# Kernel tuning notes

Hardware: AMD Instinct MI355X
Metric: run time of the kernel (lower is better)

Reference implementation:

```python
import jax, jax.numpy as jnp
import numpy as np


def l2norm(t, eps=1e-12):
    # matches F.normalize(p=2, dim=-1): divide by norm clamped to eps
    n = jnp.linalg.norm(t, axis=-1, keepdims=True)
    return t / jnp.maximum(n, eps)


def setup_inputs() -> dict:
    key = jax.random.key(0)
    kx, ke = jax.random.split(key)
    B, N, D, C = 8, 1024, 256, 8192
    x = jax.random.normal(kx, (B, N, D), dtype=jnp.float32)
    # codebook initialized l2-normalized, as in __init__ (kmeans_init=False)
    embed = l2norm(jax.random.normal(ke, (1, C, D), dtype=jnp.float32))
    return {"x": x, "embed": embed}


def reference(x, embed):
    # x: [B, N, D]; ndim < 4 -> add codebook dim h=1
    xh = x[None]                                   # [1, B, N, D]
    h, b, n, d = xh.shape
    flat = l2norm(xh.reshape(h, b * n, d))         # [1, B*N, D]
    e = l2norm(embed)                              # [1, C, D]
    # cosine-similarity distances
    dist = jnp.einsum('hnd,hcd->hnc', flat, e)     # [1, B*N, C]
    # sample_codebook_temp == 0 -> plain argmax
    idx = jnp.argmax(dist, axis=-1).reshape(h, b, n)  # [1, B, N]
    # batched_embedding: gather UN-normalized codebook rows
    quantize = jax.vmap(lambda em, ix: em[ix])(embed, idx)  # [1, B, N, D]
    # needs_codebook_dim -> strip leading dim
    return quantize[0], idx[0]
```

## Files before the change

kernel.cpp:

```cpp
#include <hip/hip_runtime.h>
#include <math.h>

#define QROWS 8192
#define DDIM  256
#define CCNT  8192
#define BM    128
#define BN    128
#define BK    32
#define CBLKS (CCNT / BN)
#define KSTEPS (DDIM / BK)

typedef __attribute__((ext_vector_type(4))) float f32x4;
typedef __attribute__((ext_vector_type(8))) short bf16x8;

__device__ __forceinline__ unsigned short f2bf(float f) {
    unsigned u = __float_as_uint(f);
    u += 0x7fffu + ((u >> 16) & 1u);
    return (unsigned short)(u >> 16);
}
__device__ __forceinline__ unsigned u32max(unsigned a, unsigned b) { return a > b ? a : b; }
__device__ __forceinline__ unsigned u32min(unsigned a, unsigned b) { return a < b ? a : b; }

__device__ __forceinline__ unsigned key32(float v, unsigned enc) {
    unsigned u = __float_as_uint(v);
    unsigned s = (unsigned)((int)u >> 31);
    return ((u ^ (s | 0x80000000u)) & 0xFFFFFF80u) | enc;
}

__global__ void k_prep_x(const float* __restrict__ x, unsigned short* __restrict__ xb) {
    const int i = (blockIdx.x * 256 + threadIdx.x) * 8;
    const float4 f0 = *reinterpret_cast<const float4*>(x + i);
    const float4 f1 = *reinterpret_cast<const float4*>(x + i + 4);
    uint4 o;
    o.x = f2bf(f0.x) | ((unsigned)f2bf(f0.y) << 16);
    o.y = f2bf(f0.z) | ((unsigned)f2bf(f0.w) << 16);
    o.z = f2bf(f1.x) | ((unsigned)f2bf(f1.y) << 16);
    o.w = f2bf(f1.z) | ((unsigned)f2bf(f1.w) << 16);
    *reinterpret_cast<uint4*>(xb + i) = o;
}

__global__ void k_prep_e(const float* __restrict__ e, unsigned short* __restrict__ eb) {
    const int row  = blockIdx.x * 4 + (threadIdx.x >> 6);
    const int lane = threadIdx.x & 63;
    const float4 v = *reinterpret_cast<const float4*>(e + (size_t)row * DDIM + lane * 4);
    float s = v.x * v.x + v.y * v.y + v.z * v.z + v.w * v.w;
    #pragma unroll
    for (int off = 1; off < 64; off <<= 1) s += __shfl_xor(s, off);
    const float inv = 1.0f / fmaxf(sqrtf(s), 1e-12f);
    ushort4 o;
    o.x = f2bf(v.x * inv); o.y = f2bf(v.y * inv);
    o.z = f2bf(v.z * inv); o.w = f2bf(v.w * inv);
    *reinterpret_cast<ushort4*>(eb + (size_t)row * DDIM + lane * 4) = o;
}

#define GLOAD_LDS(g, s) \
    __builtin_amdgcn_global_load_lds((const __attribute__((address_space(1))) void*)(g), \
                                     (__attribute__((address_space(3))) void*)(s), 16, 0, 0)

__launch_bounds__(256)
__global__ void k_gemm(const unsigned short* __restrict__ xb,
                       const unsigned short* __restrict__ eb,
                       unsigned* pout ) {
    __shared__ __align__(16) char smem[33792];

    const int tid = threadIdx.x;
    const int w = tid >> 6, l = tid & 63;
    const int wr = w >> 1, wc = w & 1;
    const int lg = l >> 4, lr = l & 15;
    const int bx = blockIdx.x, by = blockIdx.y;
    const int n0 = by * BM, c0 = bx * BN;

    const f32x4 zero = {0.f, 0.f, 0.f, 0.f};
    f32x4 acc[4][4];
    #pragma unroll
    for (int i = 0; i < 4; ++i)
        #pragma unroll
        for (int j = 0; j < 4; ++j) acc[i][j] = zero;

    const char* gA = (const char*)xb + (size_t)(n0 + (tid >> 2)) * 512 + (tid & 3) * 16;
    const char* gB = (const char*)eb + (size_t)(c0 + (tid >> 2)) * 512 + (tid & 3) * 16;
    const int wb = w * 1024;

    #define STAGE(buf, s) do {                                         \
        const int kb_ = (s) * 64;                                      \
        char* Ab_ = smem + (buf) * 8192 + wb;                          \
        char* Bb_ = smem + 16384 + (buf) * 8192 + wb;                  \
        GLOAD_LDS(gA + kb_, Ab_);                                      \
        GLOAD_LDS(gA + 64 * 512 + kb_, Ab_ + 4096);                    \
        GLOAD_LDS(gB + kb_, Bb_);                                      \
        GLOAD_LDS(gB + 64 * 512 + kb_, Bb_ + 4096);                    \
    } while (0)

    STAGE(0, 0);
    __syncthreads();

    #pragma unroll
    for (int s = 0; s < KSTEPS; ++s) {
        const int cur = s & 1;
        if (s + 1 < KSTEPS) STAGE(cur ^ 1, s + 1);

        const unsigned short* At = (const unsigned short*)(smem + cur * 8192);
        const unsigned short* Bt = (const unsigned short*)(smem + 16384 + cur * 8192);
        bf16x8 a[4], b[4];
        const int koff = lg * 8;
        #pragma unroll
        for (int mi = 0; mi < 4; ++mi)
            a[mi] = *reinterpret_cast<const bf16x8*>(&At[(wr * 64 + mi * 16 + lr) * BK + koff]);
        #pragma unroll
        for (int nj = 0; nj < 4; ++nj)
            b[nj] = *reinterpret_cast<const bf16x8*>(&Bt[(wc * 64 + nj * 16 + lr) * BK + koff]);
        #pragma unroll
        for (int mi = 0; mi < 4; ++mi)
            #pragma unroll
            for (int nj = 0; nj < 4; ++nj)
                acc[mi][nj] = __builtin_amdgcn_mfma_f32_16x16x32_bf16(a[mi], b[nj], acc[mi][nj], 0, 0, 0);
        __syncthreads();
    }

    uint2* T = (uint2*)smem;
    const unsigned encbase = (unsigned)(127 - wc * 64 - lr);
    #pragma unroll
    for (int mi = 0; mi < 4; ++mi) {
        #pragma unroll
        for (int r = 0; r < 4; ++r) {
            unsigned k0 = key32(acc[mi][0][r], encbase);
            unsigned k1 = key32(acc[mi][1][r], encbase - 16);
            unsigned k2 = key32(acc[mi][2][r], encbase - 32);
            unsigned k3 = key32(acc[mi][3][r], encbase - 48);
            const unsigned m01 = u32max(k0, k1), n01 = u32min(k0, k1);
            const unsigned m23 = u32max(k2, k3), n23 = u32min(k2, k3);
            const unsigned t1 = u32max(m01, m23);
            const unsigned t2 = u32max(u32min(m01, m23), u32max(n01, n23));
            const int rloc = wr * 64 + mi * 16 + lg * 4 + r;
            uint2 p; p.x = t1; p.y = t2;
            T[rloc * 33 + wc * 16 + lr] = p;
        }
    }
    __syncthreads();

    if (tid < BM) {
        const uint2* rp = T + tid * 33;
        unsigned T1 = 0, T2 = 0;
        #pragma unroll
        for (int i = 0; i < 32; ++i) {
            const uint2 p = rp[i];
            const unsigned n1 = u32max(T1, p.x);
            const unsigned lo = u32min(T1, p.x);
            T2 = u32max(T2, u32max(lo, p.y));
            T1 = n1;
        }
        uint2 o; o.x = T1; o.y = T2;
        *reinterpret_cast<uint2*>(pout + (size_t)(n0 + tid) * 256 + bx * 2) = o;
    }
    #undef STAGE
}

__device__ __forceinline__ unsigned long long expand_key(unsigned k, int blk) {
    const int col = blk * 128 + 127 - (int)(k & 127u);
    return ((unsigned long long)(k & 0xFFFFFF80u) << 32) | (unsigned)(~col);
}

__global__ void k_fixup(const unsigned* pk,
                        const float* __restrict__ x, const float* __restrict__ e,
                        float* out) {
    const int row = blockIdx.x;
    const int t   = threadIdx.x;
    const uint2 kv = reinterpret_cast<const uint2*>(pk + (size_t)row * 256)[t];
    unsigned long long kk0 = expand_key(kv.x, t);
    unsigned long long kk1 = expand_key(kv.y, t);

    int cand[4];
    #pragma unroll
    for (int p = 0; p < 4; ++p) {
        unsigned long long m = kk0 > kk1 ? kk0 : kk1;
        #pragma unroll
        for (int off = 1; off < 64; off <<= 1) {
            const unsigned long long o = __shfl_xor(m, off);
            if (o > m) m = o;
        }
        cand[p] = (int)(~(unsigned)m) & (CCNT - 1);
        if (kk0 == m) kk0 = 0ull;
        if (kk1 == m) kk1 = 0ull;
    }

    const float4 xv = *reinterpret_cast<const float4*>(x + (size_t)row * DDIM + t * 4);
    float best = -INFINITY; int bc = 0x7fffffff;
    #pragma unroll
    for (int p = 0; p < 4; ++p) {
        const int c = cand[p];
        const float4 ev = *reinterpret_cast<const float4*>(e + (size_t)c * DDIM + t * 4);
        float d  = xv.x * ev.x + xv.y * ev.y + xv.z * ev.z + xv.w * ev.w;
        float ss = ev.x * ev.x + ev.y * ev.y + ev.z * ev.z + ev.w * ev.w;
        #pragma unroll
        for (int off = 1; off < 64; off <<= 1) {
            d  += __shfl_xor(d, off);
            ss += __shfl_xor(ss, off);
        }
        const float v = d * (1.0f / fmaxf(sqrtf(ss), 1e-12f));
        if (v > best || (v == best && c < bc)) { best = v; bc = c; }
    }

    if (t == 0) out[(size_t)QROWS * DDIM + row] = (float)bc;
    const float4 q = *reinterpret_cast<const float4*>(e + (size_t)bc * DDIM + t * 4);
    *reinterpret_cast<float4*>(out + (size_t)row * DDIM + t * 4) = q;
}

extern "C" void kernel_launch(void* const* d_in, const int* in_sizes, int n_in,
                              void* d_out, int out_size, void* d_ws, size_t ws_size,
                              hipStream_t stream) {
    const float* x = (const float*)d_in[0];
    const float* e = (const float*)d_in[1];
    float* out = (float*)d_out;
    char* ws = (char*)d_ws;

    unsigned short* xb = (unsigned short*)ws;
    unsigned short* eb = (unsigned short*)(ws + (size_t)4 * 1024 * 1024);

    k_prep_x<<<QROWS * DDIM / (256 * 8), 256, 0, stream>>>(x, xb);
    k_prep_e<<<CCNT / 4, 256, 0, stream>>>(e, eb);
    dim3 g2(CBLKS, QROWS / BM);
    k_gemm<<<g2, 256, 0, stream>>>(xb, eb, (unsigned*)d_out);
    k_fixup<<<QROWS, 64, 0, stream>>>((const unsigned*)d_out, x, e, out);
}
```

Measured before the change: 71.41 us.

## Deepen GEMM K-tile with swizzled LDS, manual waitcnt pipeline, merge prep kernels

The GEMM now stages 64-wide K tiles with an XOR-swizzled LDS layout to avoid bank conflicts. The K loop is fully unrolled into a hand-scheduled double-buffered pipeline using explicit vmcnt/lgkmcnt waits, raw barriers and setprio around the MFMA blocks. The two prep kernels are merged into one launch, and the fixup kernel packs four rows per 256-thread block. The intent is to cut barrier count, LDS conflicts and launch overhead, at the cost of doubling LDS to 64KB, which may lower occupancy.

New measurement: 65.54 us. 8.2% less time.

```diff
diff --git a/kernel.cpp b/kernel.cpp
--- a/kernel.cpp
+++ b/kernel.cpp
@@ -6,9 +6,8 @@
 #define CCNT  8192
 #define BM    128
 #define BN    128
-#define BK    32
+#define BK    64
 #define CBLKS (CCNT / BN)
-#define KSTEPS (DDIM / BK)
 
 typedef __attribute__((ext_vector_type(4))) float f32x4;
 typedef __attribute__((ext_vector_type(8))) short bf16x8;
@@ -27,41 +26,52 @@
     return ((u ^ (s | 0x80000000u)) & 0xFFFFFF80u) | enc;
 }
 
-__global__ void k_prep_x(const float* __restrict__ x, unsigned short* __restrict__ xb) {
-    const int i = (blockIdx.x * 256 + threadIdx.x) * 8;
-    const float4 f0 = *reinterpret_cast<const float4*>(x + i);
-    const float4 f1 = *reinterpret_cast<const float4*>(x + i + 4);
-    uint4 o;
-    o.x = f2bf(f0.x) | ((unsigned)f2bf(f0.y) << 16);
-    o.y = f2bf(f0.z) | ((unsigned)f2bf(f0.w) << 16);
-    o.z = f2bf(f1.x) | ((unsigned)f2bf(f1.y) << 16);
-    o.w = f2bf(f1.z) | ((unsigned)f2bf(f1.w) << 16);
-    *reinterpret_cast<uint4*>(xb + i) = o;
-}
-
-__global__ void k_prep_e(const float* __restrict__ e, unsigned short* __restrict__ eb) {
-    const int row  = blockIdx.x * 4 + (threadIdx.x >> 6);
-    const int lane = threadIdx.x & 63;
-    const float4 v = *reinterpret_cast<const float4*>(e + (size_t)row * DDIM + lane * 4);
-    float s = v.x * v.x + v.y * v.y + v.z * v.z + v.w * v.w;
-    #pragma unroll
-    for (int off = 1; off < 64; off <<= 1) s += __shfl_xor(s, off);
-    const float inv = 1.0f / fmaxf(sqrtf(s), 1e-12f);
-    ushort4 o;
-    o.x = f2bf(v.x * inv); o.y = f2bf(v.y * inv);
-    o.z = f2bf(v.z * inv); o.w = f2bf(v.w * inv);
-    *reinterpret_cast<ushort4*>(eb + (size_t)row * DDIM + lane * 4) = o;
+__global__ void k_prep(const float* __restrict__ x, unsigned short* __restrict__ xb,
+                       const float* __restrict__ e, unsigned short* __restrict__ eb) {
+    const int bid = blockIdx.x;
+    if (bid < 1024) {
+        const int i = (bid * 256 + threadIdx.x) * 8;
+        const float4 f0 = *reinterpret_cast<const float4*>(x + i);
+        const float4 f1 = *reinterpret_cast<const float4*>(x + i + 4);
+        uint4 o;
+        o.x = f2bf(f0.x) | ((unsigned)f2bf(f0.y) << 16);
+        o.y = f2bf(f0.z) | ((unsigned)f2bf(f0.w) << 16);
+        o.z = f2bf(f1.x) | ((unsigned)f2bf(f1.y) << 16);
+        o.w = f2bf(f1.z) | ((unsigned)f2bf(f1.w) << 16);
+        *reinterpret_cast<uint4*>(xb + i) = o;
+    } else {
+        const int row  = (bid - 1024) * 4 + (threadIdx.x >> 6);
+        const int lane = threadIdx.x & 63;
+        const float4 v = *reinterpret_cast<const float4*>(e + (size_t)row * DDIM + lane * 4);
+        float s = v.x * v.x + v.y * v.y + v.z * v.z + v.w * v.w;
+        #pragma unroll
+        for (int off = 1; off < 64; off <<= 1) s += __shfl_xor(s, off);
+        const float inv = 1.0f / fmaxf(sqrtf(s), 1e-12f);
+        ushort4 o;
+        o.x = f2bf(v.x * inv); o.y = f2bf(v.y * inv);
+        o.z = f2bf(v.z * inv); o.w = f2bf(v.w * inv);
+        *reinterpret_cast<ushort4*>(eb + (size_t)row * DDIM + lane * 4) = o;
+    }
 }
 
 #define GLOAD_LDS(g, s) \
     __builtin_amdgcn_global_load_lds((const __attribute__((address_space(1))) void*)(g), \
                                      (__attribute__((address_space(3))) void*)(s), 16, 0, 0)
+
+#define SBAR do { asm volatile("" ::: "memory"); __builtin_amdgcn_s_barrier(); \
+                  asm volatile("" ::: "memory"); } while (0)
+#define WAIT_LGKM0 do { asm volatile("s_waitcnt lgkmcnt(0)" ::: "memory"); \
+                        __builtin_amdgcn_sched_barrier(0); } while (0)
+#define WAIT_VM8 do { asm volatile("s_waitcnt vmcnt(8)" ::: "memory"); \
+                      __builtin_amdgcn_sched_barrier(0); } while (0)
+#define WAIT_VM0 do { asm volatile("s_waitcnt vmcnt(0)" ::: "memory"); \
+                      __builtin_amdgcn_sched_barrier(0); } while (0)
 
 __launch_bounds__(256)
 __global__ void k_gemm(const unsigned short* __restrict__ xb,
                        const unsigned short* __restrict__ eb,
                        unsigned* pout ) {
-    __shared__ __align__(16) char smem[33792];
+    __shared__ __align__(16) char smem[65536];
 
     const int tid = threadIdx.x;
     const int w = tid >> 6, l = tid & 63;
@@ -77,45 +87,71 @@
         #pragma unroll
         for (int j = 0; j < 4; ++j) acc[i][j] = zero;
 
-    const char* gA = (const char*)xb + (size_t)(n0 + (tid >> 2)) * 512 + (tid & 3) * 16;
-    const char* gB = (const char*)eb + (size_t)(c0 + (tid >> 2)) * 512 + (tid & 3) * 16;
+    const int srow = tid >> 3;
+    const int swzp = (tid & 7) ^ (srow & 7);
+    const char* gA = (const char*)xb + (size_t)(n0 + srow) * 512 + swzp * 16;
+    const char* gB = (const char*)eb + (size_t)(c0 + srow) * 512 + swzp * 16;
     const int wb = w * 1024;
 
-    #define STAGE(buf, s) do {                                         \
-        const int kb_ = (s) * 64;                                      \
-        char* Ab_ = smem + (buf) * 8192 + wb;                          \
-        char* Bb_ = smem + 16384 + (buf) * 8192 + wb;                  \
-        GLOAD_LDS(gA + kb_, Ab_);                                      \
-        GLOAD_LDS(gA + 64 * 512 + kb_, Ab_ + 4096);                    \
-        GLOAD_LDS(gB + kb_, Bb_);                                      \
-        GLOAD_LDS(gB + 64 * 512 + kb_, Bb_ + 4096);                    \
-    } while (0)
-
-    STAGE(0, 0);
+#define STAGE(Ab, Bb, kb) do {                                          \
+    GLOAD_LDS(gA + (kb),         smem + (Ab) + 0 * 4096 + wb);          \
+    GLOAD_LDS(gA + (kb) + 16384, smem + (Ab) + 1 * 4096 + wb);          \
+    GLOAD_LDS(gA + (kb) + 32768, smem + (Ab) + 2 * 4096 + wb);          \
+    GLOAD_LDS(gA + (kb) + 49152, smem + (Ab) + 3 * 4096 + wb);          \
+    GLOAD_LDS(gB + (kb),         smem + (Bb) + 0 * 4096 + wb);          \
+    GLOAD_LDS(gB + (kb) + 16384, smem + (Bb) + 1 * 4096 + wb);          \
+    GLOAD_LDS(gB + (kb) + 32768, smem + (Bb) + 2 * 4096 + wb);          \
+    GLOAD_LDS(gB + (kb) + 49152, smem + (Bb) + 3 * 4096 + wb);          \
+} while (0)
+
+    const int aoff = (wr * 64 + lr) * 128;
+    const int boff = (wc * 64 + lr) * 128;
+    const int k0 = ((0 + lg) ^ (lr & 7)) * 16;
+    const int k1 = ((4 + lg) ^ (lr & 7)) * 16;
+
+    bf16x8 a[4][2], b[4][2];
+#define READS(Ab, Bb) do {                                                           \
+    _Pragma("unroll") for (int mi = 0; mi < 4; ++mi) {                               \
+        a[mi][0] = *reinterpret_cast<const bf16x8*>(smem + (Ab) + aoff + mi * 2048 + k0); \
+        a[mi][1] = *reinterpret_cast<const bf16x8*>(smem + (Ab) + aoff + mi * 2048 + k1); \
+    }                                                                                \
+    _Pragma("unroll") for (int nj = 0; nj < 4; ++nj) {                               \
+        b[nj][0] = *reinterpret_cast<const bf16x8*>(smem + (Bb) + boff + nj * 2048 + k0); \
+        b[nj][1] = *reinterpret_cast<const bf16x8*>(smem + (Bb) + boff + nj * 2048 + k1); \
+    }                                                                                \
+} while (0)
+
+#define MMAS() do {                                                     \
+    __builtin_amdgcn_s_setprio(1);                                      \
+    _Pragma("unroll") for (int kk = 0; kk < 2; ++kk)                    \
+      _Pragma("unroll") for (int mi = 0; mi < 4; ++mi)                  \
+        _Pragma("unroll") for (int nj = 0; nj < 4; ++nj)                \
+          acc[mi][nj] = __builtin_amdgcn_mfma_f32_16x16x32_bf16(a[mi][kk], b[nj][kk], acc[mi][nj], 0, 0, 0); \
+    __builtin_amdgcn_s_setprio(0);                                      \
+} while (0)
+
+    STAGE(0, 32768, 0);
+    STAGE(16384, 49152, 128);
+    WAIT_VM8; SBAR;
+
+    READS(0, 32768);
+    WAIT_LGKM0; SBAR;
+    STAGE(0, 32768, 256);
+    MMAS();
+    WAIT_VM8; SBAR;
+    READS(16384, 49152);
+    WAIT_LGKM0; SBAR;
+    STAGE(16384, 49152, 384);
+    MMAS();
+    WAIT_VM8; SBAR;
+    READS(0, 32768);
+    WAIT_LGKM0; SBAR;
+    MMAS();
+    WAIT_VM0; SBAR;
+    READS(16384, 49152);
+    WAIT_LGKM0;
+    MMAS();
     __syncthreads();
-
-    #pragma unroll
-    for (int s = 0; s < KSTEPS; ++s) {
-        const int cur = s & 1;
-        if (s + 1 < KSTEPS) STAGE(cur ^ 1, s + 1);
-
-        const unsigned short* At = (const unsigned short*)(smem + cur * 8192);
-        const unsigned short* Bt = (const unsigned short*)(smem + 16384 + cur * 8192);
-        bf16x8 a[4], b[4];
-        const int koff = lg * 8;
-        #pragma unroll
-        for (int mi = 0; mi < 4; ++mi)
-            a[mi] = *reinterpret_cast<const bf16x8*>(&At[(wr * 64 + mi * 16 + lr) * BK + koff]);
-        #pragma unroll
-        for (int nj = 0; nj < 4; ++nj)
-            b[nj] = *reinterpret_cast<const bf16x8*>(&Bt[(wc * 64 + nj * 16 + lr) * BK + koff]);
-        #pragma unroll
-        for (int mi = 0; mi < 4; ++mi)
-            #pragma unroll
-            for (int nj = 0; nj < 4; ++nj)
-                acc[mi][nj] = __builtin_amdgcn_mfma_f32_16x16x32_bf16(a[mi], b[nj], acc[mi][nj], 0, 0, 0);
-        __syncthreads();
-    }
 
     uint2* T = (uint2*)smem;
     const unsigned encbase = (unsigned)(127 - wc * 64 - lr);
@@ -123,12 +159,12 @@
     for (int mi = 0; mi < 4; ++mi) {
         #pragma unroll
         for (int r = 0; r < 4; ++r) {
-            unsigned k0 = key32(acc[mi][0][r], encbase);
-            unsigned k1 = key32(acc[mi][1][r], encbase - 16);
-            unsigned k2 = key32(acc[mi][2][r], encbase - 32);
-            unsigned k3 = key32(acc[mi][3][r], encbase - 48);
-            const unsigned m01 = u32max(k0, k1), n01 = u32min(k0, k1);
-            const unsigned m23 = u32max(k2, k3), n23 = u32min(k2, k3);
+            unsigned q0 = key32(acc[mi][0][r], encbase);
+            unsigned q1 = key32(acc[mi][1][r], encbase - 16);
+            unsigned q2 = key32(acc[mi][2][r], encbase - 32);
+            unsigned q3 = key32(acc[mi][3][r], encbase - 48);
+            const unsigned m01 = u32max(q0, q1), n01 = u32min(q0, q1);
+            const unsigned m23 = u32max(q2, q3), n23 = u32min(q2, q3);
             const unsigned t1 = u32max(m01, m23);
             const unsigned t2 = u32max(u32min(m01, m23), u32max(n01, n23));
             const int rloc = wr * 64 + mi * 16 + lg * 4 + r;
@@ -152,7 +188,9 @@
         uint2 o; o.x = T1; o.y = T2;
         *reinterpret_cast<uint2*>(pout + (size_t)(n0 + tid) * 256 + bx * 2) = o;
     }
-    #undef STAGE
+#undef STAGE
+#undef READS
+#undef MMAS
 }
 
 __device__ __forceinline__ unsigned long long expand_key(unsigned k, int blk) {
@@ -163,8 +201,8 @@
 __global__ void k_fixup(const unsigned* pk,
                         const float* __restrict__ x, const float* __restrict__ e,
                         float* out) {
-    const int row = blockIdx.x;
-    const int t   = threadIdx.x;
+    const int row = blockIdx.x * 4 + (threadIdx.x >> 6);
+    const int t   = threadIdx.x & 63;
     const uint2 kv = reinterpret_cast<const uint2*>(pk + (size_t)row * 256)[t];
     unsigned long long kk0 = expand_key(kv.x, t);
     unsigned long long kk1 = expand_key(kv.y, t);
@@ -216,9 +254,8 @@
     unsigned short* xb = (unsigned short*)ws;
     unsigned short* eb = (unsigned short*)(ws + (size_t)4 * 1024 * 1024);
 
-    k_prep_x<<<QROWS * DDIM / (256 * 8), 256, 0, stream>>>(x, xb);
-    k_prep_e<<<CCNT / 4, 256, 0, stream>>>(e, eb);
+    k_prep<<<3072, 256, 0, stream>>>(x, xb, e, eb);
     dim3 g2(CBLKS, QROWS / BM);
     k_gemm<<<g2, 256, 0, stream>>>(xb, eb, (unsigned*)d_out);
-    k_fixup<<<QROWS, 64, 0, stream>>>((const unsigned*)d_out, x, e, out);
-}
+    k_fixup<<<QROWS / 4, 256, 0, stream>>>((const unsigned*)d_out, x, e, out);
+}
```

## Rewrite GEMM as persistent 512x512 tiles with register-resident A and streamed top-2 reduction

Applied to the files above, without the earlier changes.

Merges the two prep kernels into one launch. Rewrites the similarity GEMM so each 512-thread block owns a 512-row panel of x and a 512-code slice of the codebook. Each wave keeps its full-depth A fragments in registers while codebook tiles stream through a 4-deep XOR-swizzled LDS ring with explicit waitcnt/barrier scheduling and setprio around the MFMAs. Top-2 keys are reduced on the fly in registers with shuffles, so the LDS epilogue goes away, and the fixup kernel packs 4 rows per block over 32 partials per row. This aims to cut global re-reads of x, launch count and epilogue overhead, at the cost of 128KB LDS, high register pressure and a coarser 8-bit column encoding that drops precision bits from the keys.

Result: faster. 67.46 us (-5.5%).

```diff
diff --git a/kernel.cpp b/kernel.cpp
--- a/kernel.cpp
+++ b/kernel.cpp
@@ -4,11 +4,6 @@
 #define QROWS 8192
 #define DDIM  256
 #define CCNT  8192
-#define BM    128
-#define BN    128
-#define BK    32
-#define CBLKS (CCNT / BN)
-#define KSTEPS (DDIM / BK)
 
 typedef __attribute__((ext_vector_type(4))) float f32x4;
 typedef __attribute__((ext_vector_type(8))) short bf16x8;
@@ -24,150 +19,191 @@
 __device__ __forceinline__ unsigned key32(float v, unsigned enc) {
     unsigned u = __float_as_uint(v);
     unsigned s = (unsigned)((int)u >> 31);
-    return ((u ^ (s | 0x80000000u)) & 0xFFFFFF80u) | enc;
-}
-
-__global__ void k_prep_x(const float* __restrict__ x, unsigned short* __restrict__ xb) {
-    const int i = (blockIdx.x * 256 + threadIdx.x) * 8;
-    const float4 f0 = *reinterpret_cast<const float4*>(x + i);
-    const float4 f1 = *reinterpret_cast<const float4*>(x + i + 4);
-    uint4 o;
-    o.x = f2bf(f0.x) | ((unsigned)f2bf(f0.y) << 16);
-    o.y = f2bf(f0.z) | ((unsigned)f2bf(f0.w) << 16);
-    o.z = f2bf(f1.x) | ((unsigned)f2bf(f1.y) << 16);
-    o.w = f2bf(f1.z) | ((unsigned)f2bf(f1.w) << 16);
-    *reinterpret_cast<uint4*>(xb + i) = o;
-}
-
-__global__ void k_prep_e(const float* __restrict__ e, unsigned short* __restrict__ eb) {
-    const int row  = blockIdx.x * 4 + (threadIdx.x >> 6);
-    const int lane = threadIdx.x & 63;
-    const float4 v = *reinterpret_cast<const float4*>(e + (size_t)row * DDIM + lane * 4);
-    float s = v.x * v.x + v.y * v.y + v.z * v.z + v.w * v.w;
-    #pragma unroll
-    for (int off = 1; off < 64; off <<= 1) s += __shfl_xor(s, off);
-    const float inv = 1.0f / fmaxf(sqrtf(s), 1e-12f);
-    ushort4 o;
-    o.x = f2bf(v.x * inv); o.y = f2bf(v.y * inv);
-    o.z = f2bf(v.z * inv); o.w = f2bf(v.w * inv);
-    *reinterpret_cast<ushort4*>(eb + (size_t)row * DDIM + lane * 4) = o;
+    return ((u ^ (s | 0x80000000u)) & 0xFFFFFF00u) | enc;
+}
+
+__global__ void k_prep(const float* __restrict__ x, unsigned short* __restrict__ xb,
+                       const float* __restrict__ e, unsigned short* __restrict__ eb) {
+    const int bid = blockIdx.x;
+    if (bid < 1024) {
+        const int i = (bid * 256 + threadIdx.x) * 8;
+        const float4 f0 = *reinterpret_cast<const float4*>(x + i);
+        const float4 f1 = *reinterpret_cast<const float4*>(x + i + 4);
+        uint4 o;
+        o.x = f2bf(f0.x) | ((unsigned)f2bf(f0.y) << 16);
+        o.y = f2bf(f0.z) | ((unsigned)f2bf(f0.w) << 16);
+        o.z = f2bf(f1.x) | ((unsigned)f2bf(f1.y) << 16);
+        o.w = f2bf(f1.z) | ((unsigned)f2bf(f1.w) << 16);
+        *reinterpret_cast<uint4*>(xb + i) = o;
+    } else {
+        const int row  = (bid - 1024) * 4 + (threadIdx.x >> 6);
+        const int lane = threadIdx.x & 63;
+        const float4 v = *reinterpret_cast<const float4*>(e + (size_t)row * DDIM + lane * 4);
+        float s = v.x * v.x + v.y * v.y + v.z * v.z + v.w * v.w;
+        #pragma unroll
+        for (int off = 1; off < 64; off <<= 1) s += __shfl_xor(s, off);
+        const float inv = 1.0f / fmaxf(sqrtf(s), 1e-12f);
+        ushort4 o;
+        o.x = f2bf(v.x * inv); o.y = f2bf(v.y * inv);
+        o.z = f2bf(v.z * inv); o.w = f2bf(v.w * inv);
+        *reinterpret_cast<ushort4*>(eb + (size_t)row * DDIM + lane * 4) = o;
+    }
 }
 
 #define GLOAD_LDS(g, s) \
     __builtin_amdgcn_global_load_lds((const __attribute__((address_space(1))) void*)(g), \
                                      (__attribute__((address_space(3))) void*)(s), 16, 0, 0)
 
-__launch_bounds__(256)
+#define SBAR do { asm volatile("" ::: "memory"); __builtin_amdgcn_s_barrier(); \
+                  asm volatile("" ::: "memory"); } while (0)
+#define WAIT_LGKM(n) do { asm volatile("s_waitcnt lgkmcnt(" #n ")" ::: "memory"); \
+                          __builtin_amdgcn_sched_barrier(0); } while (0)
+#define WAIT_VM(n) do { asm volatile("s_waitcnt vmcnt(" #n ")" ::: "memory"); \
+                        __builtin_amdgcn_sched_barrier(0); } while (0)
+
+__launch_bounds__(512, 2)
 __global__ void k_gemm(const unsigned short* __restrict__ xb,
                        const unsigned short* __restrict__ eb,
                        unsigned* pout ) {
-    __shared__ __align__(16) char smem[33792];
+    extern __shared__ char smem[];
 
     const int tid = threadIdx.x;
     const int w = tid >> 6, l = tid & 63;
-    const int wr = w >> 1, wc = w & 1;
     const int lg = l >> 4, lr = l & 15;
-    const int bx = blockIdx.x, by = blockIdx.y;
-    const int n0 = by * BM, c0 = bx * BN;
-
-    const f32x4 zero = {0.f, 0.f, 0.f, 0.f};
-    f32x4 acc[4][4];
-    #pragma unroll
-    for (int i = 0; i < 4; ++i)
-        #pragma unroll
-        for (int j = 0; j < 4; ++j) acc[i][j] = zero;
-
-    const char* gA = (const char*)xb + (size_t)(n0 + (tid >> 2)) * 512 + (tid & 3) * 16;
-    const char* gB = (const char*)eb + (size_t)(c0 + (tid >> 2)) * 512 + (tid & 3) * 16;
-    const int wb = w * 1024;
-
-    #define STAGE(buf, s) do {                                         \
-        const int kb_ = (s) * 64;                                      \
-        char* Ab_ = smem + (buf) * 8192 + wb;                          \
-        char* Bb_ = smem + 16384 + (buf) * 8192 + wb;                  \
-        GLOAD_LDS(gA + kb_, Ab_);                                      \
-        GLOAD_LDS(gA + 64 * 512 + kb_, Ab_ + 4096);                    \
-        GLOAD_LDS(gB + kb_, Bb_);                                      \
-        GLOAD_LDS(gB + 64 * 512 + kb_, Bb_ + 4096);                    \
-    } while (0)
-
-    STAGE(0, 0);
-    __syncthreads();
-
-    #pragma unroll
-    for (int s = 0; s < KSTEPS; ++s) {
-        const int cur = s & 1;
-        if (s + 1 < KSTEPS) STAGE(cur ^ 1, s + 1);
-
-        const unsigned short* At = (const unsigned short*)(smem + cur * 8192);
-        const unsigned short* Bt = (const unsigned short*)(smem + 16384 + cur * 8192);
-        bf16x8 a[4], b[4];
-        const int koff = lg * 8;
-        #pragma unroll
-        for (int mi = 0; mi < 4; ++mi)
-            a[mi] = *reinterpret_cast<const bf16x8*>(&At[(wr * 64 + mi * 16 + lr) * BK + koff]);
-        #pragma unroll
-        for (int nj = 0; nj < 4; ++nj)
-            b[nj] = *reinterpret_cast<const bf16x8*>(&Bt[(wc * 64 + nj * 16 + lr) * BK + koff]);
+    const int bid = blockIdx.x;
+    const int panel = (bid & 7) * 2 + ((bid >> 3) >> 4);
+    const int split = (bid >> 3) & 15;
+    const int n0 = panel * 512, c0 = split * 512;
+
+    const int arl = w * 2 + (l >> 5);
+    const size_t soff = (size_t)(((l & 31) ^ (arl & 7)) * 16);
+    const char* gApro = (const char*)xb + (size_t)(n0 + arl) * 512 + soff;
+    const char* gBpro = (const char*)eb + (size_t)(c0 + arl) * 512 + soff;
+    const int wlds = w * 1024;
+
+#define STAGEA(r) do { _Pragma("unroll") for (int g_ = 0; g_ < 4; ++g_)                    \
+    GLOAD_LDS(gApro + (r) * 32768 + g_ * 8192,                                             \
+              smem + ((r) & 1) * 32768 + g_ * 8192 + wlds); } while (0)
+#define STAGEB(t) do { _Pragma("unroll") for (int g_ = 0; g_ < 2; ++g_)                    \
+    GLOAD_LDS(gBpro + (size_t)(t) * 16384 + g_ * 8192,                                     \
+              smem + 65536 + ((t) & 3) * 16384 + g_ * 8192 + wlds); } while (0)
+
+    bf16x8 aF[4][8];
+#define READA(slot) do { _Pragma("unroll") for (int mi_ = 0; mi_ < 4; ++mi_)               \
+    _Pragma("unroll") for (int kk_ = 0; kk_ < 8; ++kk_)                                    \
+        aF[mi_][kk_] = *reinterpret_cast<const bf16x8*>(smem + (slot) * 32768              \
+            + (mi_ * 16 + lr) * 512 + (((kk_ * 4 + lg) ^ (lr & 7)) * 16)); } while (0)
+
+    STAGEA(0); STAGEA(1);
+    STAGEB(0); STAGEB(1); STAGEB(2); STAGEB(3);
+    WAIT_VM(12); SBAR;  if (w == 0) READA(0);  WAIT_LGKM(0); SBAR; STAGEA(2);
+    WAIT_VM(12); SBAR;  if (w == 1) READA(1);  WAIT_LGKM(0); SBAR; STAGEA(3);
+    WAIT_VM(4);  SBAR;  if (w == 2) READA(0);  WAIT_LGKM(0); SBAR; STAGEA(4);
+    WAIT_VM(4);  SBAR;  if (w == 3) READA(1);  WAIT_LGKM(0); SBAR; STAGEA(5);
+    WAIT_VM(4);  SBAR;  if (w == 4) READA(0);  WAIT_LGKM(0); SBAR; STAGEA(6);
+    WAIT_VM(4);  SBAR;  if (w == 5) READA(1);  WAIT_LGKM(0); SBAR; STAGEA(7);
+    WAIT_VM(4);  SBAR;  if (w == 6) READA(0);  WAIT_LGKM(0); SBAR;
+    WAIT_VM(0);  SBAR;  if (w == 7) READA(1);  WAIT_LGKM(0); SBAR;
+
+    const f32x4 zf4 = {0.f, 0.f, 0.f, 0.f};
+    f32x4 acc[4][2];
+    #pragma unroll
+    for (int i = 0; i < 4; ++i) { acc[i][0] = zf4; acc[i][1] = zf4; }
+    unsigned rk1[16], rk2[16];
+    #pragma unroll
+    for (int i = 0; i < 16; ++i) { rk1[i] = 0u; rk2[i] = 0u; }
+    bf16x8 bF[2][2];
+    const int bcol0 = lr * 512;
+    const int cxor = lr & 7;
+
+#define FLUSH(half) do {                                                                   \
+    _Pragma("unroll") for (int i_ = 0; i_ < 16; ++i_) {                                    \
+        unsigned t1_ = rk1[i_], t2_ = rk2[i_];                                             \
+        _Pragma("unroll") for (int off_ = 1; off_ < 16; off_ <<= 1) {                      \
+            const unsigned o1_ = __shfl_xor(t1_, off_);                                    \
+            const unsigned o2_ = __shfl_xor(t2_, off_);                                    \
+            const unsigned n1_ = u32max(t1_, o1_), lo_ = u32min(t1_, o1_);                 \
+            t2_ = u32max(u32max(t2_, o2_), lo_);                                           \
+            t1_ = n1_;                                                                     \
+        }                                                                                  \
+        if (lr == 0) {                                                                     \
+            const int row_ = n0 + w * 64 + (i_ >> 2) * 16 + lg * 4 + (i_ & 3);             \
+            uint2 o_; o_.x = t1_; o_.y = t2_;                                              \
+            *reinterpret_cast<uint2*>(pout + (size_t)row_ * 256 + split * 4 + (half) * 2) = o_; \
+        }                                                                                  \
+        rk1[i_] = 0u; rk2[i_] = 0u;                                                        \
+    }                                                                                      \
+} while (0)
+
+    #pragma unroll 1
+    for (int t = 0; t < 16; ++t) {
+        const char* sb = smem + 65536 + (t & 3) * 16384;
+        #pragma unroll
+        for (int nj = 0; nj < 2; ++nj)
+            bF[0][nj] = *reinterpret_cast<const bf16x8*>(sb + nj * 8192 + bcol0 + ((lg ^ cxor) * 16));
+        #pragma unroll
+        for (int kk = 0; kk < 8; ++kk) {
+            if (kk < 7) {
+                #pragma unroll
+                for (int nj = 0; nj < 2; ++nj)
+                    bF[(kk + 1) & 1][nj] = *reinterpret_cast<const bf16x8*>(
+                        sb + nj * 8192 + bcol0 + ((((kk + 1) * 4 + lg) ^ cxor) * 16));
+                WAIT_LGKM(2);
+            } else {
+                WAIT_LGKM(0);
+            }
+            __builtin_amdgcn_s_setprio(1);
+            #pragma unroll
+            for (int mi = 0; mi < 4; ++mi)
+                #pragma unroll
+                for (int nj = 0; nj < 2; ++nj)
+                    acc[mi][nj] = __builtin_amdgcn_mfma_f32_16x16x32_bf16(
+                        aF[mi][kk], bF[kk & 1][nj], acc[mi][nj], 0, 0, 0);
+            __builtin_amdgcn_s_setprio(0);
+        }
+        SBAR;
+        if (t < 12) STAGEB(t + 4);
+
+        const unsigned encb = (unsigned)(255 - (t & 7) * 32) - (unsigned)lr;
         #pragma unroll
         for (int mi = 0; mi < 4; ++mi)
             #pragma unroll
-            for (int nj = 0; nj < 4; ++nj)
-                acc[mi][nj] = __builtin_amdgcn_mfma_f32_16x16x32_bf16(a[mi], b[nj], acc[mi][nj], 0, 0, 0);
-        __syncthreads();
-    }
-
-    uint2* T = (uint2*)smem;
-    const unsigned encbase = (unsigned)(127 - wc * 64 - lr);
-    #pragma unroll
-    for (int mi = 0; mi < 4; ++mi) {
-        #pragma unroll
-        for (int r = 0; r < 4; ++r) {
-            unsigned k0 = key32(acc[mi][0][r], encbase);
-            unsigned k1 = key32(acc[mi][1][r], encbase - 16);
-            unsigned k2 = key32(acc[mi][2][r], encbase - 32);
-            unsigned k3 = key32(acc[mi][3][r], encbase - 48);
-            const unsigned m01 = u32max(k0, k1), n01 = u32min(k0, k1);
-            const unsigned m23 = u32max(k2, k3), n23 = u32min(k2, k3);
-            const unsigned t1 = u32max(m01, m23);
-            const unsigned t2 = u32max(u32min(m01, m23), u32max(n01, n23));
-            const int rloc = wr * 64 + mi * 16 + lg * 4 + r;
-            uint2 p; p.x = t1; p.y = t2;
-            T[rloc * 33 + wc * 16 + lr] = p;
-        }
-    }
-    __syncthreads();
-
-    if (tid < BM) {
-        const uint2* rp = T + tid * 33;
-        unsigned T1 = 0, T2 = 0;
-        #pragma unroll
-        for (int i = 0; i < 32; ++i) {
-            const uint2 p = rp[i];
-            const unsigned n1 = u32max(T1, p.x);
-            const unsigned lo = u32min(T1, p.x);
-            T2 = u32max(T2, u32max(lo, p.y));
-            T1 = n1;
-        }
-        uint2 o; o.x = T1; o.y = T2;
-        *reinterpret_cast<uint2*>(pout + (size_t)(n0 + tid) * 256 + bx * 2) = o;
-    }
-    #undef STAGE
-}
-
-__device__ __forceinline__ unsigned long long expand_key(unsigned k, int blk) {
-    const int col = blk * 128 + 127 - (int)(k & 127u);
-    return ((unsigned long long)(k & 0xFFFFFF80u) << 32) | (unsigned)(~col);
+            for (int rr = 0; rr < 4; ++rr) {
+                const unsigned q0 = key32(acc[mi][0][rr], encb);
+                const unsigned q1 = key32(acc[mi][1][rr], encb - 16u);
+                const unsigned m01 = u32max(q0, q1), n01 = u32min(q0, q1);
+                const int i = mi * 4 + rr;
+                const unsigned lo = u32min(rk1[i], m01);
+                rk1[i] = u32max(rk1[i], m01);
+                rk2[i] = u32max(u32max(rk2[i], n01), lo);
+                acc[mi][0][rr] = 0.0f; acc[mi][1][rr] = 0.0f;
+            }
+        if (t == 7) FLUSH(0);
+        if (t == 15) FLUSH(1);
+        if (t < 15) {
+            if (t < 12) { WAIT_VM(6); } else { WAIT_VM(0); }
+            SBAR;
+        }
+    }
+#undef STAGEA
+#undef STAGEB
+#undef READA
+#undef FLUSH
 }
 
 __global__ void k_fixup(const unsigned* pk,
                         const float* __restrict__ x, const float* __restrict__ e,
                         float* out) {
-    const int row = blockIdx.x;
-    const int t   = threadIdx.x;
-    const uint2 kv = reinterpret_cast<const uint2*>(pk + (size_t)row * 256)[t];
-    unsigned long long kk0 = expand_key(kv.x, t);
-    unsigned long long kk1 = expand_key(kv.y, t);
+    const int row = blockIdx.x * 4 + (threadIdx.x >> 6);
+    const int t   = threadIdx.x & 63;
+    unsigned long long kk0 = 0ull, kk1 = 0ull;
+    if (t < 32) {
+        const uint2 kv = reinterpret_cast<const uint2*>(pk + (size_t)row * 256)[t];
+        const int col0 = t * 256 + 255 - (int)(kv.x & 255u);
+        kk0 = ((unsigned long long)(kv.x & 0xFFFFFF00u) << 32) | (unsigned)(~col0);
+        const int col1 = t * 256 + 255 - (int)(kv.y & 255u);
+        kk1 = ((unsigned long long)(kv.y & 0xFFFFFF00u) << 32) | (unsigned)(~col1);
+    }
 
     int cand[4];
     #pragma unroll
@@ -216,9 +252,10 @@
     unsigned short* xb = (unsigned short*)ws;
     unsigned short* eb = (unsigned short*)(ws + (size_t)4 * 1024 * 1024);
 
-    k_prep_x<<<QROWS * DDIM / (256 * 8), 256, 0, stream>>>(x, xb);
-    k_prep_e<<<CCNT / 4, 256, 0, stream>>>(e, eb);
-    dim3 g2(CBLKS, QROWS / BM);
-    k_gemm<<<g2, 256, 0, stream>>>(xb, eb, (unsigned*)d_out);
-    k_fixup<<<QROWS, 64, 0, stream>>>((const unsigned*)d_out, x, e, out);
-}
+    hipFuncSetAttribute(reinterpret_cast<const void*>(k_gemm),
+                        hipFuncAttributeMaxDynamicSharedMemorySize, 131072);
+
+    k_prep<<<3072, 256, 0, stream>>>(x, xb, e, eb);
+    k_gemm<<<256, 512, 131072, stream>>>(xb, eb, (unsigned*)d_out);
+    k_fixup<<<QROWS / 4, 256, 0, stream>>>((const unsigned*)d_out, x, e, out);
+}
```
